# Kernel optimization log

Hardware: AMD Instinct MI355X
Metric: run time of the kernel (lower is better)

The kernel has to match this reference:

```python
import jax, jax.numpy as jnp
import numpy as np

C_IN, D_STATE, EXPAND, KS = 64, 16, 2, 3
D_INNER = EXPAND * C_IN
HP_KS, HP_SIGMA = 15, 3.0
B, H, W = 4, 256, 256


def _gauss2d(ks, sigma):
    ax = jnp.arange(ks, dtype=jnp.float32) - (ks - 1) / 2.0
    g = jnp.exp(-(ax ** 2) / (2.0 * sigma ** 2))
    g = g / g.sum()
    return jnp.outer(g, g)


def _dwconv(x, w, pad):
    # x: [B,d,H,W], w: [d,1,kh,kw] depthwise
    return jax.lax.conv_general_dilated(
        x, w, window_strides=(1, 1), padding=[(pad, pad), (pad, pad)],
        dimension_numbers=("NCHW", "OIHW", "NCHW"),
        feature_group_count=x.shape[1])


def _selective_scan(u, dt, Bm, Cm, A, D, scan_axis):
    # u, dt: [B,d,H,W]; Bm, Cm: [B,N,H,W]; scan over scan_axis (2 or 3)
    u_s = jnp.moveaxis(u, scan_axis, 0)    # [L,B,d,M]
    dt_s = jnp.moveaxis(dt, scan_axis, 0)
    B_s = jnp.moveaxis(Bm, scan_axis, 0)   # [L,B,N,M]
    C_s = jnp.moveaxis(Cm, scan_axis, 0)
    Bb, d = u.shape[0], u.shape[1]
    M = u_s.shape[-1]
    N = A.shape[1]

    def step(h, inp):
        uj, dtj, Bj, Cj = inp                     # [B,d,M], [B,d,M], [B,N,M], [B,N,M]
        expA = jnp.exp(dtj[..., None] * A[None, :, None, :])   # [B,d,M,N]
        Bt = jnp.transpose(Bj, (0, 2, 1))[:, None]              # [B,1,M,N]
        Ct = jnp.transpose(Cj, (0, 2, 1))[:, None]
        h = expA * h + (uj * dtj)[..., None] * Bt               # [B,d,M,N]
        y = jnp.sum(h * Ct, axis=-1) + D[None, :, None] * uj    # [B,d,M]
        return h, y

    h0 = jnp.zeros((Bb, d, M, N), u.dtype)
    _, ys = jax.lax.scan(step, h0, (u_s, dt_s, B_s, C_s))
    return jnp.moveaxis(ys, 0, scan_axis)


def setup_inputs() -> dict:
    key = jax.random.key(0)
    ks = jax.random.split(key, 12)
    d, N = D_INNER, D_STATE
    A_log = -(jnp.linspace(0.0, 1.0, N, dtype=jnp.float32) * jnp.log(10.0))
    A_log = jnp.broadcast_to(A_log[None, :], (d, N)).astype(jnp.float32)
    return {
        "x": jax.random.normal(ks[0], (B, C_IN, H, W), jnp.float32),
        "in_proj_w": jax.random.normal(ks[1], (2 * d, C_IN), jnp.float32) * 0.05,
        "in_proj_b": jnp.zeros((2 * d,), jnp.float32),
        "dw_w": jax.random.normal(ks[2], (d, 1, KS, KS), jnp.float32) * 0.2,
        "dw_b": jnp.zeros((d,), jnp.float32),
        "xproj_w": jax.random.normal(ks[3], (1 + 2 * N, d), jnp.float32) * 0.05,
        "dtproj_w": jax.random.normal(ks[4], (d, 1), jnp.float32) * 0.5,
        "dtproj_b": jax.random.normal(ks[5], (d,), jnp.float32) * 0.5 - 4.0,
        "A_log": A_log,
        "D": jnp.ones((d,), jnp.float32),
        "out_w": jax.random.normal(ks[6], (C_IN, d), jnp.float32) * 0.05,
        "out_b": jnp.zeros((C_IN,), jnp.float32),
    }


def reference(x, in_proj_w, in_proj_b, dw_w, dw_b, xproj_w,
              dtproj_w, dtproj_b, A_log, D, out_w, out_b):
    d, N = D_INNER, D_STATE
    # in_proj (1x1 conv)
    uz = jnp.einsum("bchw,oc->bohw", x, in_proj_w) + in_proj_b[None, :, None, None]
    U, Z = uz[:, :d], uz[:, d:]
    # depthwise conv
    Uc = _dwconv(U, dw_w, KS // 2) + dw_b[None, :, None, None]
    # tanh(alpha * x) * weight + bias with alpha=0.5, weight=1, bias=0
    Uc = jnp.tanh(0.5 * Uc)
    # Gaussian high-pass: x - depthwise gaussian blur
    g = _gauss2d(HP_KS, HP_SIGMA)
    gk = jnp.broadcast_to(g[None, None], (d, 1, HP_KS, HP_KS))
    Uc = Uc - _dwconv(Uc, gk, HP_KS // 2)
    # x_proj (1x1 conv, no bias)
    params = jnp.einsum("bchw,oc->bohw", Uc, xproj_w)
    delta_in = params[:, :1]                 # [B,1,H,W]
    B_map = params[:, 1:1 + N]               # [B,N,H,W]
    C_map = params[:, 1 + N:1 + 2 * N]
    dt = jax.nn.softplus(jnp.einsum("bohw,do->bdhw", delta_in, dtproj_w)
                         + dtproj_b[None, :, None, None])
    A = -jnp.exp(A_log)
    Y_h = _selective_scan(Uc, dt, B_map, C_map, A, D, scan_axis=3)   # scan over W
    Y_v = _selective_scan(Y_h, dt, B_map, C_map, A, D, scan_axis=2)  # scan over H
    out = Y_v * jax.nn.sigmoid(Z)
    return jnp.einsum("bdhw,cd->bchw", out, out_w) + out_b[None, :, None, None]
```

## Files before the change

kernel.cpp:

```cpp
#include <hip/hip_runtime.h>
#include <hip/hip_bf16.h>
#include <math.h>

#define BB 4
#define CIN 64
#define DI 128
#define NS 16
#define HH 256
#define WW 256
#define HW 65536
#define NCH_P 33

__device__ __forceinline__ float softplusf(float x) {
    return fmaxf(x, 0.f) + __logf(1.0f + __expf(-fabsf(x)));
}
__device__ __forceinline__ float tanh_half(float a) {
    return 1.0f - 2.0f / (1.0f + __expf(a));
}
__device__ __forceinline__ float sigmoidf(float z) {
    return 1.0f / (1.0f + __expf(-z));
}

__device__ __forceinline__ void gauss15(float* g) {
    float s = 0.f;
#pragma unroll
    for (int i = 0; i < 15; ++i) {
        float a = (float)i - 7.0f;
        g[i] = __expf(-a * a / 18.0f);
        s += g[i];
    }
    float inv = 1.0f / s;
#pragma unroll
    for (int i = 0; i < 15; ++i) g[i] *= inv;
}

__global__ __launch_bounds__(256) void k_inproj(
    const float* __restrict__ xb, const float* __restrict__ w,
    const float* __restrict__ bias, float* __restrict__ Ub) {
    int p = blockIdx.x * 256 + threadIdx.x;
    float xv[CIN];
#pragma unroll
    for (int c = 0; c < CIN; ++c) xv[c] = xb[(size_t)c * HW + p];
    for (int o = 0; o < DI; ++o) {
        float acc = bias[o];
        const float* wr = w + o * CIN;
#pragma unroll
        for (int c = 0; c < CIN; ++c) acc = fmaf(xv[c], wr[c], acc);
        Ub[(size_t)o * HW + p] = acc;
    }
}

#define TILE_H 16
__global__ __launch_bounds__(256) void k_conv(
    const float* __restrict__ Ub, const float* __restrict__ dww,
    const float* __restrict__ dwb, float* __restrict__ Ucb) {
    __shared__ float sU[32 * 256];
    __shared__ float sC[30 * 272];
    int c  = blockIdx.x >> 4;
    int t  = blockIdx.x & 15;
    int h0 = t * TILE_H;
    int w  = threadIdx.x;

    const float* base = Ub + (size_t)c * HW;
#pragma unroll
    for (int i = 0; i < 32; ++i) {
        int hh = h0 + i - 8;
        sU[i * 256 + w] = (hh >= 0 && hh < HH) ? base[hh * WW + w] : 0.f;
    }
    __syncthreads();

    float wt[9];
#pragma unroll
    for (int i = 0; i < 9; ++i) wt[i] = dww[c * 9 + i];
    float bb = dwb[c];

#pragma unroll
    for (int i = 0; i < 30; ++i) {
        int r = h0 + i - 7;
        float v = 0.f;
        if (r >= 0 && r < HH) {
            float acc = bb;
#pragma unroll
            for (int ky = 0; ky < 3; ++ky) {
                const float* ur = sU + (i + ky) * 256;
#pragma unroll
                for (int kx = 0; kx < 3; ++kx) {
                    int ww = w + kx - 1;
                    if (ww >= 0 && ww < WW) acc = fmaf(ur[ww], wt[ky * 3 + kx], acc);
                }
            }
            v = tanh_half(acc);
        }
        sC[i * 272 + w + 7] = v;
    }
    if (w < 7) {
#pragma unroll
        for (int i = 0; i < 30; ++i) { sC[i * 272 + w] = 0.f; sC[i * 272 + w + 263] = 0.f; }
    }
    __syncthreads();

    float g[15]; gauss15(g);
#pragma unroll
    for (int i = 0; i < 30; ++i) {
        float acc = 0.f;
#pragma unroll
        for (int k = 0; k < 15; ++k) acc = fmaf(sC[i * 272 + w + k], g[k], acc);
        sU[i * 256 + w] = acc;
    }
    float* outp = Ucb + (size_t)c * HW + h0 * WW + w;
#pragma unroll
    for (int i = 0; i < TILE_H; ++i) {
        float acc = 0.f;
#pragma unroll
        for (int k = 0; k < 15; ++k) acc = fmaf(sU[(i + k) * 256 + w], g[k], acc);
        float center = sC[(i + 7) * 272 + w + 7];
        outp[i * WW] = center - acc;
    }
}

__global__ __launch_bounds__(256) void k_xproj(
    const float* __restrict__ Uc, const float* __restrict__ xw,
    float* __restrict__ P) {
    int p = blockIdx.x * 256 + threadIdx.x;
    int b = p >> 16;
    int rem = p & 65535;
    const float* up = Uc + (size_t)b * DI * HW + rem;
    float acc[NCH_P];
#pragma unroll
    for (int o = 0; o < NCH_P; ++o) acc[o] = 0.f;
    for (int c = 0; c < DI; ++c) {
        float u = up[(size_t)c * HW];
#pragma unroll
        for (int o = 0; o < NCH_P; ++o) acc[o] = fmaf(u, xw[o * DI + c], acc[o]);
    }
    float* pp = P + (size_t)b * NCH_P * HW + rem;
#pragma unroll
    for (int o = 0; o < NCH_P; ++o) pp[(size_t)o * HW] = acc[o];
}

#define CW 32
__global__ __launch_bounds__(128) void k_scan_w(
    float* __restrict__ UY, const float* __restrict__ P,
    const float* __restrict__ A_log, const float* __restrict__ dtw,
    const float* __restrict__ dtb, const float* __restrict__ Dv) {
    __shared__ float sU[DI * 33];
    __shared__ float sP[CW * 36];
    int bh = blockIdx.x;
    int b = bh >> 8;
    int h = bh & 255;
    int t = threadIdx.x;

    float Av[NS];
#pragma unroll
    for (int n = 0; n < NS; ++n) Av[n] = -__expf(A_log[t * NS + n]);
    float wdt = dtw[t], bdt = dtb[t], Dd = Dv[t];
    float hS[NS];
#pragma unroll
    for (int n = 0; n < NS; ++n) hS[n] = 0.f;

    float* ubase = UY + (size_t)(b * DI) * HW + (size_t)h * WW;
    const float* prow = P + (size_t)(b * NCH_P) * HW + (size_t)h * WW;

    const int w4 = (t & 7) * 4;
    const int dbase = t >> 3;

    float4 rU[8];
    float rP[9];
#pragma unroll
    for (int p = 0; p < 8; ++p)
        rU[p] = *(const float4*)(ubase + (size_t)(dbase + p * 16) * HW + w4);
#pragma unroll
    for (int i = 0; i < 9; ++i) {
        int idx = i * 128 + t, ch = idx >> 5, wi = idx & 31;
        rP[i] = (ch < NCH_P) ? prow[(size_t)ch * HW + wi] : 0.f;
    }

    for (int w0 = 0; w0 < WW; w0 += CW) {
#pragma unroll
        for (int p = 0; p < 8; ++p) {
            float* s = sU + (dbase + p * 16) * 33 + w4;
            s[0] = rU[p].x; s[1] = rU[p].y; s[2] = rU[p].z; s[3] = rU[p].w;
        }
#pragma unroll
        for (int i = 0; i < 9; ++i) {
            int idx = i * 128 + t, ch = idx >> 5, wi = idx & 31;
            if (ch < NCH_P) sP[wi * 36 + ch] = rP[i];
        }
        __syncthreads();
        if (w0 + CW < WW) {
#pragma unroll
            for (int p = 0; p < 8; ++p)
                rU[p] = *(const float4*)(ubase + (size_t)(dbase + p * 16) * HW + w0 + CW + w4);
#pragma unroll
            for (int i = 0; i < 9; ++i) {
                int idx = i * 128 + t, ch = idx >> 5, wi = idx & 31;
                rP[i] = (ch < NCH_P) ? prow[(size_t)ch * HW + w0 + CW + wi] : 0.f;
            }
        }
#pragma unroll 2
        for (int wi = 0; wi < CW; ++wi) {
            const float* pr = sP + wi * 36;
            float4 q0 = *(const float4*)(pr);
            float4 q1 = *(const float4*)(pr + 4);
            float4 q2 = *(const float4*)(pr + 8);
            float4 q3 = *(const float4*)(pr + 12);
            float4 q4 = *(const float4*)(pr + 16);
            float4 q5 = *(const float4*)(pr + 20);
            float4 q6 = *(const float4*)(pr + 24);
            float4 q7 = *(const float4*)(pr + 28);
            float q8 = pr[32];
            float u = sU[t * 33 + wi];
            float dt = softplusf(fmaf(q0.x, wdt, bdt));
            float ud = u * dt;
            float y = Dd * u;
            float Bv[NS] = {q0.y,q0.z,q0.w,q1.x,q1.y,q1.z,q1.w,q2.x,
                            q2.y,q2.z,q2.w,q3.x,q3.y,q3.z,q3.w,q4.x};
            float Cv[NS] = {q4.y,q4.z,q4.w,q5.x,q5.y,q5.z,q5.w,q6.x,
                            q6.y,q6.z,q6.w,q7.x,q7.y,q7.z,q7.w,q8};
#pragma unroll
            for (int n = 0; n < NS; ++n) {
                float e = __expf(dt * Av[n]);
                hS[n] = fmaf(e, hS[n], ud * Bv[n]);
                y = fmaf(hS[n], Cv[n], y);
            }
            sU[t * 33 + wi] = y;
        }
        __syncthreads();
#pragma unroll
        for (int p = 0; p < 8; ++p) {
            const float* s = sU + (dbase + p * 16) * 33 + w4;
            float4 v; v.x = s[0]; v.y = s[1]; v.z = s[2]; v.w = s[3];
            *(float4*)(ubase + (size_t)(dbase + p * 16) * HW + w0 + w4) = v;
        }
        __syncthreads();
    }
}

__global__ __launch_bounds__(256) void k_scan_h(
    float* __restrict__ UY, const float* __restrict__ P,
    const float* __restrict__ A_log, const float* __restrict__ dtw,
    const float* __restrict__ dtb, const float* __restrict__ Dv) {
    int bd = blockIdx.x;
    int b = bd >> 7;
    int d = bd & (DI - 1);
    int w = threadIdx.x;
    float Av[NS];
#pragma unroll
    for (int n = 0; n < NS; ++n) Av[n] = -__expf(A_log[d * NS + n]);
    float wdt = dtw[d], bdt = dtb[d], Dd = Dv[d];
    float* ucol = UY + (size_t)bd * HW + w;
    const float* pcol = P + (size_t)(b * NCH_P) * HW + w;
    float hS[NS];
#pragma unroll
    for (int n = 0; n < NS; ++n) hS[n] = 0.f;

    float uA, deA, BA[NS], CA[NS];
    float uB, deB, Bb[NS], Cb[NS];
    uA = ucol[0]; deA = pcol[0];
#pragma unroll
    for (int n = 0; n < NS; ++n) { BA[n] = pcol[(size_t)(1 + n) * HW]; CA[n] = pcol[(size_t)(17 + n) * HW]; }
    uB = ucol[WW]; deB = pcol[WW];
#pragma unroll
    for (int n = 0; n < NS; ++n) { Bb[n] = pcol[(size_t)(1 + n) * HW + WW]; Cb[n] = pcol[(size_t)(17 + n) * HW + WW]; }

    for (int h = 0; h < HH; h += 2) {
        size_t o2 = (size_t)min(h + 2, HH - 1) * WW;
        size_t o3 = (size_t)min(h + 3, HH - 1) * WW;
        float u2 = ucol[o2], de2 = pcol[o2];
        float u3 = ucol[o3], de3 = pcol[o3];
        float B2[NS], C2[NS], B3[NS], C3[NS];
#pragma unroll
        for (int n = 0; n < NS; ++n) {
            B2[n] = pcol[(size_t)(1 + n) * HW + o2];
            C2[n] = pcol[(size_t)(17 + n) * HW + o2];
            B3[n] = pcol[(size_t)(1 + n) * HW + o3];
            C3[n] = pcol[(size_t)(17 + n) * HW + o3];
        }
        {
            float dt = softplusf(fmaf(deA, wdt, bdt));
            float ud = uA * dt;
            float y = Dd * uA;
#pragma unroll
            for (int n = 0; n < NS; ++n) {
                float e = __expf(dt * Av[n]);
                hS[n] = fmaf(e, hS[n], ud * BA[n]);
                y = fmaf(hS[n], CA[n], y);
            }
            ucol[(size_t)h * WW] = y;
        }
        {
            float dt = softplusf(fmaf(deB, wdt, bdt));
            float ud = uB * dt;
            float y = Dd * uB;
#pragma unroll
            for (int n = 0; n < NS; ++n) {
                float e = __expf(dt * Av[n]);
                hS[n] = fmaf(e, hS[n], ud * Bb[n]);
                y = fmaf(hS[n], Cb[n], y);
            }
            ucol[(size_t)(h + 1) * WW] = y;
        }
        uA = u2; deA = de2; uB = u3; deB = de3;
#pragma unroll
        for (int n = 0; n < NS; ++n) { BA[n] = B2[n]; CA[n] = C2[n]; Bb[n] = B3[n]; Cb[n] = C3[n]; }
    }
}

__global__ __launch_bounds__(256) void k_out(
    const float* __restrict__ Y, const float* __restrict__ xb,
    const float* __restrict__ wz, const float* __restrict__ bz,
    const float* __restrict__ ow, const float* __restrict__ ob,
    float* __restrict__ outb) {
    int p = blockIdx.x * 256 + threadIdx.x;
    int b = p >> 16;
    int rem = p & 65535;
    const float* yp = Y + (size_t)b * DI * HW + rem;
    const float* xp = xb + (size_t)b * CIN * HW + rem;
    float xv[CIN];
#pragma unroll
    for (int c = 0; c < CIN; ++c) xv[c] = xp[(size_t)c * HW];
    float acc[CIN];
#pragma unroll
    for (int c = 0; c < CIN; ++c) acc[c] = 0.f;
    for (int dd = 0; dd < DI; ++dd) {
        float yv = yp[(size_t)dd * HW];
        float z = bz[dd];
        const float* wr = wz + dd * CIN;
#pragma unroll
        for (int c = 0; c < CIN; ++c) z = fmaf(xv[c], wr[c], z);
        float gate = yv * sigmoidf(z);
#pragma unroll
        for (int c = 0; c < CIN; ++c) acc[c] = fmaf(gate, ow[c * DI + dd], acc[c]);
    }
    float* op = outb + (size_t)b * CIN * HW + rem;
#pragma unroll
    for (int c = 0; c < CIN; ++c) op[(size_t)c * HW] = acc[c] + ob[c];
}

extern "C" void kernel_launch(void* const* d_in, const int* in_sizes, int n_in,
                              void* d_out, int out_size, void* d_ws, size_t ws_size,
                              hipStream_t stream) {
    const float* x     = (const float*)d_in[0];
    const float* ipw   = (const float*)d_in[1];
    const float* ipb   = (const float*)d_in[2];
    const float* dww   = (const float*)d_in[3];
    const float* dwb   = (const float*)d_in[4];
    const float* xpw   = (const float*)d_in[5];
    const float* dtw   = (const float*)d_in[6];
    const float* dtb   = (const float*)d_in[7];
    const float* A_log = (const float*)d_in[8];
    const float* Dv    = (const float*)d_in[9];
    const float* ow    = (const float*)d_in[10];
    const float* ob    = (const float*)d_in[11];
    float* out = (float*)d_out;

    const float* wz = ipw + (size_t)DI * CIN;
    const float* bz = ipb + DI;

    const size_t PLANE = (size_t)DI * HW;
    const size_t NB    = (size_t)BB * PLANE;

    if (ws_size >= (NB + PLANE) * sizeof(float)) {
        float* bufY = (float*)d_ws;
        float* bufU = bufY + NB;
        float* P    = out;
        for (int b = 0; b < BB; ++b) {
            k_inproj<<<HW / 256, 256, 0, stream>>>(x + (size_t)b * CIN * HW, ipw, ipb, bufU);
            k_conv<<<DI * 16, 256, 0, stream>>>(bufU, dww, dwb, bufY + (size_t)b * PLANE);
        }
        k_xproj<<<BB * (HW / 256), 256, 0, stream>>>(bufY, xpw, P);
        k_scan_w<<<BB * HH, 128, 0, stream>>>(bufY, P, A_log, dtw, dtb, Dv);
        k_scan_h<<<BB * DI, 256, 0, stream>>>(bufY, P, A_log, dtw, dtb, Dv);
        k_out<<<BB * (HW / 256), 256, 0, stream>>>(bufY, x, wz, bz, ow, ob, out);
    } else {
        float* bufA = (float*)d_ws;
        float* bufY = bufA + PLANE;
        for (int b = 0; b < BB; ++b) {
            const float* xb = x + (size_t)b * CIN * HW;
            k_inproj<<<HW / 256, 256, 0, stream>>>(xb, ipw, ipb, bufA);
            k_conv<<<DI * 16, 256, 0, stream>>>(bufA, dww, dwb, bufY);
            k_xproj<<<HW / 256, 256, 0, stream>>>(bufY, xpw, bufA);
            k_scan_w<<<HH, 128, 0, stream>>>(bufY, bufA, A_log, dtw, dtb, Dv);
            k_scan_h<<<DI, 256, 0, stream>>>(bufY, bufA, A_log, dtw, dtb, Dv);
            k_out<<<HW / 256, 256, 0, stream>>>(bufY, xb, wz, bz, ow, ob, out + (size_t)b * CIN * HW);
        }
    }
}
```

Baseline: 1.801 ms.

## Split output kernel into gate and projection, widen inproj grid

The in-projection kernel now launches two blocks along y, each covering 64 output channels, so there are twice as many blocks per batch. Its dot product is split over four accumulators to shorten the FMA dependency chain. The fused output kernel is split into a gating kernel, which writes Y*sigmoid(z) back in place, and a separate 128-to-64 projection kernel, which lowers per-thread register pressure. The split costs an extra full read and write of the 128-channel buffer through global memory.

```diff
diff --git a/kernel.cpp b/kernel.cpp
--- a/kernel.cpp
+++ b/kernel.cpp
@@ -38,15 +38,22 @@
     const float* __restrict__ xb, const float* __restrict__ w,
     const float* __restrict__ bias, float* __restrict__ Ub) {
     int p = blockIdx.x * 256 + threadIdx.x;
+    int og = blockIdx.y * 64;
     float xv[CIN];
 #pragma unroll
     for (int c = 0; c < CIN; ++c) xv[c] = xb[(size_t)c * HW + p];
-    for (int o = 0; o < DI; ++o) {
-        float acc = bias[o];
+#pragma unroll 2
+    for (int o = og; o < og + 64; ++o) {
+        float a0 = bias[o], a1 = 0.f, a2 = 0.f, a3 = 0.f;
         const float* wr = w + o * CIN;
 #pragma unroll
-        for (int c = 0; c < CIN; ++c) acc = fmaf(xv[c], wr[c], acc);
-        Ub[(size_t)o * HW + p] = acc;
+        for (int c = 0; c < CIN; c += 4) {
+            a0 = fmaf(xv[c],     wr[c],     a0);
+            a1 = fmaf(xv[c + 1], wr[c + 1], a1);
+            a2 = fmaf(xv[c + 2], wr[c + 2], a2);
+            a3 = fmaf(xv[c + 3], wr[c + 3], a3);
+        }
+        Ub[(size_t)o * HW + p] = (a0 + a1) + (a2 + a3);
     }
 }
 
@@ -306,33 +313,50 @@
     }
 }
 
-__global__ __launch_bounds__(256) void k_out(
-    const float* __restrict__ Y, const float* __restrict__ xb,
-    const float* __restrict__ wz, const float* __restrict__ bz,
-    const float* __restrict__ ow, const float* __restrict__ ob,
-    float* __restrict__ outb) {
+__global__ __launch_bounds__(256) void k_gate(
+    float* __restrict__ Y, const float* __restrict__ x,
+    const float* __restrict__ wz, const float* __restrict__ bz) {
     int p = blockIdx.x * 256 + threadIdx.x;
     int b = p >> 16;
     int rem = p & 65535;
-    const float* yp = Y + (size_t)b * DI * HW + rem;
-    const float* xp = xb + (size_t)b * CIN * HW + rem;
+    const float* xp = x + (size_t)b * CIN * HW + rem;
     float xv[CIN];
 #pragma unroll
     for (int c = 0; c < CIN; ++c) xv[c] = xp[(size_t)c * HW];
+    float* yp = Y + (size_t)b * DI * HW + rem;
+#pragma unroll 2
+    for (int dd = 0; dd < DI; ++dd) {
+        float z0 = 0.f, z1 = 0.f, z2 = 0.f, z3 = 0.f;
+        const float* wr = wz + dd * CIN;
+#pragma unroll
+        for (int c = 0; c < CIN; c += 4) {
+            z0 = fmaf(xv[c],     wr[c],     z0);
+            z1 = fmaf(xv[c + 1], wr[c + 1], z1);
+            z2 = fmaf(xv[c + 2], wr[c + 2], z2);
+            z3 = fmaf(xv[c + 3], wr[c + 3], z3);
+        }
+        float z = bz[dd] + ((z0 + z1) + (z2 + z3));
+        float yv = yp[(size_t)dd * HW];
+        yp[(size_t)dd * HW] = yv * sigmoidf(z);
+    }
+}
+
+__global__ __launch_bounds__(256) void k_out2(
+    const float* __restrict__ G, const float* __restrict__ ow,
+    const float* __restrict__ ob, float* __restrict__ outp) {
+    int p = blockIdx.x * 256 + threadIdx.x;
+    int b = p >> 16;
+    int rem = p & 65535;
+    const float* gp = G + (size_t)b * DI * HW + rem;
     float acc[CIN];
 #pragma unroll
     for (int c = 0; c < CIN; ++c) acc[c] = 0.f;
     for (int dd = 0; dd < DI; ++dd) {
-        float yv = yp[(size_t)dd * HW];
-        float z = bz[dd];
-        const float* wr = wz + dd * CIN;
-#pragma unroll
-        for (int c = 0; c < CIN; ++c) z = fmaf(xv[c], wr[c], z);
-        float gate = yv * sigmoidf(z);
-#pragma unroll
-        for (int c = 0; c < CIN; ++c) acc[c] = fmaf(gate, ow[c * DI + dd], acc[c]);
-    }
-    float* op = outb + (size_t)b * CIN * HW + rem;
+        float g = gp[(size_t)dd * HW];
+#pragma unroll
+        for (int c = 0; c < CIN; ++c) acc[c] = fmaf(g, ow[c * DI + dd], acc[c]);
+    }
+    float* op = outp + (size_t)b * CIN * HW + rem;
 #pragma unroll
     for (int c = 0; c < CIN; ++c) op[(size_t)c * HW] = acc[c] + ob[c];
 }
@@ -365,24 +389,26 @@
         float* bufU = bufY + NB;
         float* P    = out;
         for (int b = 0; b < BB; ++b) {
-            k_inproj<<<HW / 256, 256, 0, stream>>>(x + (size_t)b * CIN * HW, ipw, ipb, bufU);
+            k_inproj<<<dim3(HW / 256, 2), 256, 0, stream>>>(x + (size_t)b * CIN * HW, ipw, ipb, bufU);
             k_conv<<<DI * 16, 256, 0, stream>>>(bufU, dww, dwb, bufY + (size_t)b * PLANE);
         }
         k_xproj<<<BB * (HW / 256), 256, 0, stream>>>(bufY, xpw, P);
         k_scan_w<<<BB * HH, 128, 0, stream>>>(bufY, P, A_log, dtw, dtb, Dv);
         k_scan_h<<<BB * DI, 256, 0, stream>>>(bufY, P, A_log, dtw, dtb, Dv);
-        k_out<<<BB * (HW / 256), 256, 0, stream>>>(bufY, x, wz, bz, ow, ob, out);
+        k_gate<<<BB * (HW / 256), 256, 0, stream>>>(bufY, x, wz, bz);
+        k_out2<<<BB * (HW / 256), 256, 0, stream>>>(bufY, ow, ob, out);
     } else {
         float* bufA = (float*)d_ws;
         float* bufY = bufA + PLANE;
         for (int b = 0; b < BB; ++b) {
             const float* xb = x + (size_t)b * CIN * HW;
-            k_inproj<<<HW / 256, 256, 0, stream>>>(xb, ipw, ipb, bufA);
+            k_inproj<<<dim3(HW / 256, 2), 256, 0, stream>>>(xb, ipw, ipb, bufA);
             k_conv<<<DI * 16, 256, 0, stream>>>(bufA, dww, dwb, bufY);
             k_xproj<<<HW / 256, 256, 0, stream>>>(bufY, xpw, bufA);
             k_scan_w<<<HH, 128, 0, stream>>>(bufY, bufA, A_log, dtw, dtb, Dv);
             k_scan_h<<<DI, 256, 0, stream>>>(bufY, bufA, A_log, dtw, dtb, Dv);
-            k_out<<<HW / 256, 256, 0, stream>>>(bufY, xb, wz, bz, ow, ob, out + (size_t)b * CIN * HW);
-        }
-    }
-}
+            k_gate<<<HW / 256, 256, 0, stream>>>(bufY, xb, wz, bz);
+            k_out2<<<HW / 256, 256, 0, stream>>>(bufY, ow, ob, out + (size_t)b * CIN * HW);
+        }
+    }
+}
```

After: 1.551 ms. -13.9%, faster.
